# Optimization experiments

Hardware: AMD Instinct MI355X
Metric: run time of the kernel (lower is better)

## Reference

```python
import jax, jax.numpy as jnp
import numpy as np
from jax import lax

B, D, H = 8192, 128, 512   # batch of initial conditions, state dim, MLP width
NSTEPS = 64                # fixed Tsit5 micro-steps over [t0, t1]

# Tsit5 Butcher tableau (Tsitouras 2011), 5th-order solution weights.
A21 = 0.161
A31, A32 = -0.008480655492356989, 0.335480655492357
A41, A42, A43 = 2.8971530571054935, -6.359448489975075, 4.3622954328695815
A51, A52, A53, A54 = 5.325864828439257, -11.748883564062828, 7.4955393428898365, -0.09249506636175525
A61, A62, A63, A64, A65 = 5.86145544294642, -12.92096931784711, 8.159367898576159, -0.071584973281401, -0.028269050394068383
B1, B2, B3, B4, B5, B6 = 0.09646076681806523, 0.01, 0.4798896504144996, 1.379008574103742, -3.290069515436081, 2.324710524099774


def setup_inputs() -> dict:
    key = jax.random.key(0)
    ks = jax.random.split(key, 8)
    s1 = 1.0 / np.sqrt(D)
    s2 = 1.0 / np.sqrt(H)
    return {
        "y0": jax.random.normal(ks[0], (B, D), dtype=jnp.float32),
        "ts": jnp.arange(2, dtype=jnp.float32),  # [0., 1.]
        "W1": jax.random.normal(ks[1], (D, H), dtype=jnp.float32) * s1,
        "b1": jnp.zeros((H,), dtype=jnp.float32),
        "W2": jax.random.normal(ks[2], (H, H), dtype=jnp.float32) * s2,
        "b2": jnp.zeros((H,), dtype=jnp.float32),
        "W3": jax.random.normal(ks[3], (H, D), dtype=jnp.float32) * s2,
        "b3": jnp.zeros((D,), dtype=jnp.float32),
    }


def _mlp(y, W1, b1, W2, b2, W3, b3):
    # autonomous dynamics: f(t, x) = MLP(x)  (t is ignored, as in Dynamics.__call__)
    h = jnp.tanh(y @ W1 + b1)
    h = jnp.tanh(h @ W2 + b2)
    return h @ W3 + b3


def reference(y0, ts, W1, b1, W2, b2, W3, b3):
    dt = (ts[-1] - ts[0]) / NSTEPS
    f = lambda y: _mlp(y, W1, b1, W2, b2, W3, b3)

    def step(y, _):
        k1 = f(y)
        k2 = f(y + dt * (A21 * k1))
        k3 = f(y + dt * (A31 * k1 + A32 * k2))
        k4 = f(y + dt * (A41 * k1 + A42 * k2 + A43 * k3))
        k5 = f(y + dt * (A51 * k1 + A52 * k2 + A53 * k3 + A54 * k4))
        k6 = f(y + dt * (A61 * k1 + A62 * k2 + A63 * k3 + A64 * k4 + A65 * k5))
        y_new = y + dt * (B1 * k1 + B2 * k2 + B3 * k3 + B4 * k4 + B5 * k5 + B6 * k6)
        return y_new, None

    yT, _ = lax.scan(step, y0, None, length=NSTEPS)
    return yT  # solution.ys[-1]: state at t1, shape [B, D]
```

## Files before the change

### kernel.cpp

```cpp
#include <hip/hip_runtime.h>
#include <hip/hip_bf16.h>


#define NSTEPS 64

typedef __attribute__((ext_vector_type(8))) short short8;
typedef __attribute__((ext_vector_type(16))) float f32x16;

static constexpr int OFF_YT   = 0;
static constexpr int OFF_H    = 8192;
static constexpr int KO_S     = 129;
static constexpr int K_BYTES  = 32 * KO_S * 4;
static constexpr int OFF_K0   = 8192 + 32768;
static constexpr int OFF_BIAS = OFF_K0 + 5 * K_BYTES;
static constexpr int SMEM_BYTES = OFF_BIAS + 1152 * 4;

#define C_A21 0.161f
#define C_A31 (-0.008480655492356989f)
#define C_A32 0.335480655492357f
#define C_A41 2.8971530571054935f
#define C_A42 (-6.359448489975075f)
#define C_A43 4.3622954328695815f
#define C_A51 5.325864828439257f
#define C_A52 (-11.748883564062828f)
#define C_A53 7.4955393428898365f
#define C_A54 (-0.09249506636175525f)
#define C_A61 5.86145544294642f
#define C_A62 (-12.92096931784711f)
#define C_A63 8.159367898576159f
#define C_A64 (-0.071584973281401f)
#define C_A65 (-0.028269050394068383f)
#define C_B1 0.09646076681806523f
#define C_B2 0.01f
#define C_B3 0.4798896504144996f
#define C_B4 1.379008574103742f
#define C_B5 (-3.290069515436081f)
#define C_B6 2.324710524099774f

__device__ __forceinline__ float fast_tanh(float x) {
    float e = __builtin_amdgcn_exp2f(x * 2.88539008177792681472f);
    return 1.0f - 2.0f * __builtin_amdgcn_rcpf(e + 1.0f);
}

__device__ __forceinline__ unsigned int pack2(float a, float b) {
    unsigned short lo = __builtin_bit_cast(unsigned short, __float2bfloat16(a));
    unsigned short hi = __builtin_bit_cast(unsigned short, __float2bfloat16(b));
    return ((unsigned int)hi << 16) | (unsigned int)lo;
}

#define MFMA(a, b, c) __builtin_amdgcn_mfma_f32_32x32x16_bf16((a), (b), (c), 0, 0, 0)

__device__ __forceinline__ void store_h(char* smem, int dstOff, const f32x16& acc,
                                        int mt, int q, int lm, const float* bias) {
#pragma unroll
    for (int gblk = 0; gblk < 4; ++gblk) {
        const int r0   = gblk * 4;
        const int row0 = 8 * (r0 >> 2) + 4 * q;
        const int m0   = mt * 32 + row0;
        float v0 = fast_tanh(acc[r0]     + bias[m0]);
        float v1 = fast_tanh(acc[r0 + 1] + bias[m0 + 1]);
        float v2 = fast_tanh(acc[r0 + 2] + bias[m0 + 2]);
        float v3 = fast_tanh(acc[r0 + 3] + bias[m0 + 3]);
        uint2 dw;
        dw.x = pack2(v0, v1);
        dw.y = pack2(v2, v3);
        const int b  = 2 * mt + (r0 >> 3);
        const int s  = lm + 32 * ((r0 >> 2) & 1);
        const int sp = (s + b) & 63;
        *(uint2*)(smem + dstOff + (b << 10) + (sp << 4) + (q << 3)) = dw;
    }
}

__device__ __forceinline__ void write_ytmp(char* smem, int tid, const float* v) {
    const int b  = (tid & 15) >> 1;
    const int s  = (tid >> 4) + 32 * (tid & 1);
    const int sp = (s + b) & 63;
    uint4 pk;
    pk.x = pack2(v[0], v[1]);
    pk.y = pack2(v[2], v[3]);
    pk.z = pack2(v[4], v[5]);
    pk.w = pack2(v[6], v[7]);
    *(uint4*)(smem + OFF_YT + (b << 10) + (sp << 4)) = pk;
}

__device__ __forceinline__ void read_k(const char* smem, int koOff, int tid, float* k) {
    const float* ko = (const float*)(smem + koOff);
    const int kb = (tid >> 4) * KO_S + (tid & 15) * 8;
#pragma unroll
    for (int i = 0; i < 8; ++i) k[i] = ko[kb + i];
}

__device__ __forceinline__ void mlp_eval(char* smem, const uint4* __restrict__ wp,
                                         int tid, int koOff) {
    const int l  = tid & 63;
    const int w  = tid >> 6;
    const int q  = l >> 5;
    const int lm = l & 31;
    const float* sb = (const float*)(smem + OFF_BIAS);

    __syncthreads();

    {
        f32x16 acc0, acc1;
#pragma unroll
        for (int i = 0; i < 16; ++i) { acc0[i] = 0.f; acc1[i] = 0.f; }
        const int mt0 = 2 * w, mt1 = mt0 + 1;
#pragma unroll
        for (int kc = 0; kc < 8; ++kc) {
            short8 bf = *(const short8*)(smem + OFF_YT + (kc << 10) + (((l + kc) & 63) << 4));
            uint4 a0 = wp[(mt0 * 8 + kc) * 64 + l];
            uint4 a1 = wp[(mt1 * 8 + kc) * 64 + l];
            acc0 = MFMA(__builtin_bit_cast(short8, a0), bf, acc0);
            acc1 = MFMA(__builtin_bit_cast(short8, a1), bf, acc1);
        }
        store_h(smem, OFF_H, acc0, mt0, q, lm, sb);
        store_h(smem, OFF_H, acc1, mt1, q, lm, sb);
    }
    __syncthreads();

    {
        f32x16 acc0, acc1;
#pragma unroll
        for (int i = 0; i < 16; ++i) { acc0[i] = 0.f; acc1[i] = 0.f; }
        const int mt0 = 2 * w, mt1 = mt0 + 1;
#pragma unroll 4
        for (int kc = 0; kc < 32; ++kc) {
            short8 bf = *(const short8*)(smem + OFF_H + (kc << 10) + (((l + kc) & 63) << 4));
            uint4 a0 = wp[8192 + (mt0 * 32 + kc) * 64 + l];
            uint4 a1 = wp[8192 + (mt1 * 32 + kc) * 64 + l];
            acc0 = MFMA(__builtin_bit_cast(short8, a0), bf, acc0);
            acc1 = MFMA(__builtin_bit_cast(short8, a1), bf, acc1);
        }
        __syncthreads();
        store_h(smem, OFF_H, acc0, mt0, q, lm, sb + 512);
        store_h(smem, OFF_H, acc1, mt1, q, lm, sb + 512);
    }
    __syncthreads();

    {
        f32x16 acc;
#pragma unroll
        for (int i = 0; i < 16; ++i) acc[i] = 0.f;
        const int mt  = w & 3;
        const int kc0 = (w >> 2) * 16;
#pragma unroll 4
        for (int kk = 0; kk < 16; ++kk) {
            const int kc = kc0 + kk;
            short8 bf = *(const short8*)(smem + OFF_H + (kc << 10) + (((l + kc) & 63) << 4));
            uint4 a = wp[40960 + (mt * 32 + kc) * 64 + l];
            acc = MFMA(__builtin_bit_cast(short8, a), bf, acc);
        }
        float* ko = (float*)(smem + koOff);
        if (w < 4) {
#pragma unroll
            for (int r = 0; r < 16; ++r) {
                const int row = (r & 3) + 8 * (r >> 2) + 4 * q;
                const int df  = mt * 32 + row;
                ko[lm * KO_S + df] = acc[r] + sb[1024 + df];
            }
        }
        __syncthreads();
        if (w >= 4) {
#pragma unroll
            for (int r = 0; r < 16; ++r) {
                const int row = (r & 3) + 8 * (r >> 2) + 4 * q;
                const int df  = mt * 32 + row;
                ko[lm * KO_S + df] += acc[r];
            }
        }
        __syncthreads();
    }
}

__global__ __launch_bounds__(512, 1) void ode_kernel(
    const float* __restrict__ y0, const float* __restrict__ ts,
    const float* __restrict__ b1, const float* __restrict__ b2,
    const float* __restrict__ b3, const uint4* __restrict__ wp,
    float* __restrict__ yout)
{
    extern __shared__ __align__(16) char smem[];
    const int tid = threadIdx.x;
    const int g   = blockIdx.x;

    {
        float* sb = (float*)(smem + OFF_BIAS);
        for (int i = tid; i < 1152; i += 512) {
            float v = (i < 512) ? b1[i] : ((i < 1024) ? b2[i - 512] : b3[i - 1024]);
            sb[i] = v;
        }
    }

    const int row = g * 32 + (tid >> 4);
    const int c0  = (tid & 15) * 8;
    float y[8];
    {
        const float4* src = (const float4*)(y0 + row * 128 + c0);
        float4 v0 = src[0], v1 = src[1];
        y[0] = v0.x; y[1] = v0.y; y[2] = v0.z; y[3] = v0.w;
        y[4] = v1.x; y[5] = v1.y; y[6] = v1.z; y[7] = v1.w;
    }

    const float dt = __builtin_bit_cast(float, __builtin_amdgcn_readfirstlane(
        __builtin_bit_cast(int, (ts[1] - ts[0]) * (1.0f / (float)NSTEPS))));

    float yn[8], yt[8];

    for (int step = 0; step < NSTEPS; ++step) {

        write_ytmp(smem, tid, y);
        mlp_eval(smem, wp, tid, OFF_K0);
        {
            float k1[8];
            read_k(smem, OFF_K0, tid, k1);
#pragma unroll
            for (int i = 0; i < 8; ++i) {
                yn[i] = fmaf(dt, C_B1 * k1[i], y[i]);
                yt[i] = fmaf(dt, C_A21 * k1[i], y[i]);
            }
        }

        write_ytmp(smem, tid, yt);
        mlp_eval(smem, wp, tid, OFF_K0 + K_BYTES);
        {
            float k1[8], k2[8];
            read_k(smem, OFF_K0, tid, k1);
            read_k(smem, OFF_K0 + K_BYTES, tid, k2);
#pragma unroll
            for (int i = 0; i < 8; ++i) {
                yn[i] = fmaf(dt, C_B2 * k2[i], yn[i]);
                yt[i] = fmaf(dt, fmaf(C_A32, k2[i], C_A31 * k1[i]), y[i]);
            }
        }

        write_ytmp(smem, tid, yt);
        mlp_eval(smem, wp, tid, OFF_K0 + 2 * K_BYTES);
        {
            float k1[8], k2[8], k3[8];
            read_k(smem, OFF_K0, tid, k1);
            read_k(smem, OFF_K0 + K_BYTES, tid, k2);
            read_k(smem, OFF_K0 + 2 * K_BYTES, tid, k3);
#pragma unroll
            for (int i = 0; i < 8; ++i) {
                yn[i] = fmaf(dt, C_B3 * k3[i], yn[i]);
                yt[i] = fmaf(dt, fmaf(C_A43, k3[i],
                             fmaf(C_A42, k2[i], C_A41 * k1[i])), y[i]);
            }
        }

        write_ytmp(smem, tid, yt);
        mlp_eval(smem, wp, tid, OFF_K0 + 3 * K_BYTES);
        {
            float k1[8], k2[8], k3[8], k4[8];
            read_k(smem, OFF_K0, tid, k1);
            read_k(smem, OFF_K0 + K_BYTES, tid, k2);
            read_k(smem, OFF_K0 + 2 * K_BYTES, tid, k3);
            read_k(smem, OFF_K0 + 3 * K_BYTES, tid, k4);
#pragma unroll
            for (int i = 0; i < 8; ++i) {
                yn[i] = fmaf(dt, C_B4 * k4[i], yn[i]);
                yt[i] = fmaf(dt, fmaf(C_A54, k4[i], fmaf(C_A53, k3[i],
                             fmaf(C_A52, k2[i], C_A51 * k1[i]))), y[i]);
            }
        }

        write_ytmp(smem, tid, yt);
        mlp_eval(smem, wp, tid, OFF_K0 + 4 * K_BYTES);
        {
            float k1[8], k2[8], k3[8], k4[8], k5[8];
            read_k(smem, OFF_K0, tid, k1);
            read_k(smem, OFF_K0 + K_BYTES, tid, k2);
            read_k(smem, OFF_K0 + 2 * K_BYTES, tid, k3);
            read_k(smem, OFF_K0 + 3 * K_BYTES, tid, k4);
            read_k(smem, OFF_K0 + 4 * K_BYTES, tid, k5);
#pragma unroll
            for (int i = 0; i < 8; ++i) {
                yn[i] = fmaf(dt, C_B5 * k5[i], yn[i]);
                yt[i] = fmaf(dt, fmaf(C_A65, k5[i], fmaf(C_A64, k4[i],
                             fmaf(C_A63, k3[i], fmaf(C_A62, k2[i],
                             C_A61 * k1[i])))), y[i]);
            }
        }

        write_ytmp(smem, tid, yt);
        mlp_eval(smem, wp, tid, OFF_K0);
        {
            float k6[8];
            read_k(smem, OFF_K0, tid, k6);
#pragma unroll
            for (int i = 0; i < 8; ++i) {
                y[i] = fmaf(dt, C_B6 * k6[i], yn[i]);
            }
        }
    }

    {
        float4 o0, o1;
        o0.x = y[0]; o0.y = y[1]; o0.z = y[2]; o0.w = y[3];
        o1.x = y[4]; o1.y = y[5]; o1.z = y[6]; o1.w = y[7];
        float4* dst = (float4*)(yout + row * 128 + c0);
        dst[0] = o0; dst[1] = o1;
    }
}

__global__ void pack_weights(const float* __restrict__ W1, const float* __restrict__ W2,
                             const float* __restrict__ W3, unsigned short* __restrict__ out)
{
    const int tid = blockIdx.x * blockDim.x + threadIdx.x;
    float v;
    if (tid < 65536) {
        const int e = tid, blk = e >> 9, wi = e & 511, l = wi >> 3, j = wi & 7;
        const int mt = blk >> 3, kc = blk & 7;
        const int m = mt * 32 + (l & 31);
        const int k = kc * 16 + 8 * (l >> 5) + j;
        v = W1[k * 512 + m];
    } else if (tid < 327680) {
        const int e = tid - 65536, blk = e >> 9, wi = e & 511, l = wi >> 3, j = wi & 7;
        const int mt = blk >> 5, kc = blk & 31;
        const int m = mt * 32 + (l & 31);
        const int k = kc * 16 + 8 * (l >> 5) + j;
        v = W2[k * 512 + m];
    } else {
        const int e = tid - 327680, blk = e >> 9, wi = e & 511, l = wi >> 3, j = wi & 7;
        const int mt = blk >> 5, kc = blk & 31;
        const int m = mt * 32 + (l & 31);
        const int k = kc * 16 + 8 * (l >> 5) + j;
        v = W3[k * 128 + m];
    }
    out[tid] = __builtin_bit_cast(unsigned short, __float2bfloat16(v));
}

extern "C" void kernel_launch(void* const* d_in, const int* in_sizes, int n_in,
                              void* d_out, int out_size, void* d_ws, size_t ws_size,
                              hipStream_t stream)
{
    const float* y0 = (const float*)d_in[0];
    const float* ts = (const float*)d_in[1];
    const float* W1 = (const float*)d_in[2];
    const float* b1 = (const float*)d_in[3];
    const float* W2 = (const float*)d_in[4];
    const float* b2 = (const float*)d_in[5];
    const float* W3 = (const float*)d_in[6];
    const float* b3 = (const float*)d_in[7];
    unsigned short* wp = (unsigned short*)d_ws;

    pack_weights<<<1536, 256, 0, stream>>>(W1, W2, W3, wp);

    (void)hipFuncSetAttribute((const void*)ode_kernel,
                              hipFuncAttributeMaxDynamicSharedMemorySize, SMEM_BYTES);
    ode_kernel<<<256, 512, SMEM_BYTES, stream>>>(y0, ts, b1, b2, b3,
                                                 (const uint4*)wp, (float*)d_out);
}
```

Measured before the change: 3.567 ms.

## Stream MLP weights via async global-to-LDS DMA with a cross-layer double-buffered pipeline

Weight fragments are no longer loaded from global memory straight into registers right before each MFMA. Each wave now issues global_load_lds DMAs into a private double-buffered LDS staging area, two k-chunks ahead, and the prefetch chain continues across layer boundaries and into the next MLP evaluation. This is meant to hide global/L2 latency behind MFMA work. The __syncthreads calls are replaced by manual lgkmcnt waits plus s_barrier, and the explicit vmcnt/lgkmcnt waits must be exactly right or the code will read stale staging data.

```diff
diff --git a/kernel.cpp b/kernel.cpp
--- a/kernel.cpp
+++ b/kernel.cpp
@@ -13,7 +13,18 @@
 static constexpr int K_BYTES  = 32 * KO_S * 4;
 static constexpr int OFF_K0   = 8192 + 32768;
 static constexpr int OFF_BIAS = OFF_K0 + 5 * K_BYTES;
-static constexpr int SMEM_BYTES = OFF_BIAS + 1152 * 4;
+static constexpr int OFF_ST   = OFF_BIAS + 1152 * 4;
+static constexpr int SMEM_BYTES = OFF_ST + 8 * 4096;
+
+#define W1B(mt, kc) ((mt) * 8 + (kc))
+#define W2B(mt, kc) (128 + (mt) * 32 + (kc))
+#define W3B(mt, kc) (640 + (mt) * 32 + (kc))
+
+#define VMCNT2() asm volatile("s_waitcnt vmcnt(2)" ::: "memory")
+#define VMCNT0() asm volatile("s_waitcnt vmcnt(0)" ::: "memory")
+#define LGKM0()  asm volatile("s_waitcnt lgkmcnt(0)" ::: "memory")
+#define HBAR()   do { LGKM0(); __builtin_amdgcn_s_barrier(); \
+                      asm volatile("" ::: "memory"); } while (0)
 
 #define C_A21 0.161f
 #define C_A31 (-0.008480655492356989f)
@@ -50,6 +61,12 @@
 
 #define MFMA(a, b, c) __builtin_amdgcn_mfma_f32_32x32x16_bf16((a), (b), (c), 0, 0, 0)
 
+__device__ __forceinline__ void dma16(const uint4* __restrict__ g, char* s_) {
+    __builtin_amdgcn_global_load_lds(
+        (const __attribute__((address_space(1))) void*)g,
+        (__attribute__((address_space(3))) void*)s_, 16, 0, 0);
+}
+
 __device__ __forceinline__ void store_h(char* smem, int dstOff, const f32x16& acc,
                                         int mt, int q, int lm, const float* bias) {
 #pragma unroll
@@ -90,85 +107,140 @@
     for (int i = 0; i < 8; ++i) k[i] = ko[kb + i];
 }
 
+#define LD_YT(kc) (*(const short8*)(smem + OFF_YT + ((kc) << 10) + (((l + (kc)) & 63) << 4)))
+#define LD_H(kc)  (*(const short8*)(smem + OFF_H  + ((kc) << 10) + (((l + (kc)) & 63) << 4)))
+
 __device__ __forceinline__ void mlp_eval(char* smem, const uint4* __restrict__ wp,
                                          int tid, int koOff) {
-    const int l  = tid & 63;
-    const int w  = tid >> 6;
-    const int q  = l >> 5;
-    const int lm = l & 31;
+    const int l   = tid & 63;
+    const int w   = tid >> 6;
+    const int q   = l >> 5;
+    const int lm  = l & 31;
+    const int mt0 = 2 * w, mt1 = mt0 + 1;
+    const int mt3 = w & 3, kc03 = (w >> 2) * 16;
     const float* sb = (const float*)(smem + OFF_BIAS);
-
-    __syncthreads();
+    char* stw = smem + OFF_ST + (w << 12);
+
+    HBAR();
+
+    uint4 a0c, a1c, a0n, a1n;
+    short8 bc, bn, b0c, b1c, b0n, b1n;
 
     {
         f32x16 acc0, acc1;
 #pragma unroll
         for (int i = 0; i < 16; ++i) { acc0[i] = 0.f; acc1[i] = 0.f; }
-        const int mt0 = 2 * w, mt1 = mt0 + 1;
-#pragma unroll
-        for (int kc = 0; kc < 8; ++kc) {
-            short8 bf = *(const short8*)(smem + OFF_YT + (kc << 10) + (((l + kc) & 63) << 4));
-            uint4 a0 = wp[(mt0 * 8 + kc) * 64 + l];
-            uint4 a1 = wp[(mt1 * 8 + kc) * 64 + l];
-            acc0 = MFMA(__builtin_bit_cast(short8, a0), bf, acc0);
-            acc1 = MFMA(__builtin_bit_cast(short8, a1), bf, acc1);
+        VMCNT2();
+        a0c = *(const uint4*)(stw + (l << 4));
+        a1c = *(const uint4*)(stw + 1024 + (l << 4));
+        bc  = LD_YT(0);
+#pragma unroll
+        for (int s = 0; s < 8; ++s) {
+            LGKM0();
+            char* ibuf = stw + ((s & 1) << 11);
+            if (s < 6) {
+                dma16(wp + W1B(mt0, s + 2) * 64 + l, ibuf);
+                dma16(wp + W1B(mt1, s + 2) * 64 + l, ibuf + 1024);
+            } else {
+                dma16(wp + W2B(mt0, s - 6) * 64 + l, ibuf);
+                dma16(wp + W2B(mt1, s - 6) * 64 + l, ibuf + 1024);
+            }
+            VMCNT2();
+            char* rbuf = stw + (((s + 1) & 1) << 11);
+            a0n = *(const uint4*)(rbuf + (l << 4));
+            a1n = *(const uint4*)(rbuf + 1024 + (l << 4));
+            if (s < 7) bn = LD_YT(s + 1);
+            acc0 = MFMA(__builtin_bit_cast(short8, a0c), bc, acc0);
+            acc1 = MFMA(__builtin_bit_cast(short8, a1c), bc, acc1);
+            a0c = a0n; a1c = a1n; bc = bn;
         }
         store_h(smem, OFF_H, acc0, mt0, q, lm, sb);
         store_h(smem, OFF_H, acc1, mt1, q, lm, sb);
     }
-    __syncthreads();
+    HBAR();
 
     {
         f32x16 acc0, acc1;
 #pragma unroll
         for (int i = 0; i < 16; ++i) { acc0[i] = 0.f; acc1[i] = 0.f; }
-        const int mt0 = 2 * w, mt1 = mt0 + 1;
+        bc = LD_H(0);
 #pragma unroll 4
-        for (int kc = 0; kc < 32; ++kc) {
-            short8 bf = *(const short8*)(smem + OFF_H + (kc << 10) + (((l + kc) & 63) << 4));
-            uint4 a0 = wp[8192 + (mt0 * 32 + kc) * 64 + l];
-            uint4 a1 = wp[8192 + (mt1 * 32 + kc) * 64 + l];
-            acc0 = MFMA(__builtin_bit_cast(short8, a0), bf, acc0);
-            acc1 = MFMA(__builtin_bit_cast(short8, a1), bf, acc1);
-        }
-        __syncthreads();
+        for (int s2 = 0; s2 < 32; ++s2) {
+            LGKM0();
+            char* ibuf = stw + ((s2 & 1) << 11);
+            if (s2 < 30) {
+                dma16(wp + W2B(mt0, s2 + 2) * 64 + l, ibuf);
+                dma16(wp + W2B(mt1, s2 + 2) * 64 + l, ibuf + 1024);
+            } else {
+                const int j = 2 * (s2 - 30);
+                dma16(wp + W3B(mt3, kc03 + j)     * 64 + l, ibuf);
+                dma16(wp + W3B(mt3, kc03 + j + 1) * 64 + l, ibuf + 1024);
+            }
+            VMCNT2();
+            char* rbuf = stw + (((s2 + 1) & 1) << 11);
+            a0n = *(const uint4*)(rbuf + (l << 4));
+            a1n = *(const uint4*)(rbuf + 1024 + (l << 4));
+            if (s2 < 31) bn = LD_H(s2 + 1);
+            acc0 = MFMA(__builtin_bit_cast(short8, a0c), bc, acc0);
+            acc1 = MFMA(__builtin_bit_cast(short8, a1c), bc, acc1);
+            a0c = a0n; a1c = a1n; bc = bn;
+        }
+        HBAR();
         store_h(smem, OFF_H, acc0, mt0, q, lm, sb + 512);
         store_h(smem, OFF_H, acc1, mt1, q, lm, sb + 512);
     }
-    __syncthreads();
+    HBAR();
 
     {
         f32x16 acc;
 #pragma unroll
         for (int i = 0; i < 16; ++i) acc[i] = 0.f;
-        const int mt  = w & 3;
-        const int kc0 = (w >> 2) * 16;
-#pragma unroll 4
-        for (int kk = 0; kk < 16; ++kk) {
-            const int kc = kc0 + kk;
-            short8 bf = *(const short8*)(smem + OFF_H + (kc << 10) + (((l + kc) & 63) << 4));
-            uint4 a = wp[40960 + (mt * 32 + kc) * 64 + l];
-            acc = MFMA(__builtin_bit_cast(short8, a), bf, acc);
+        b0c = LD_H(kc03);
+        b1c = LD_H(kc03 + 1);
+#pragma unroll
+        for (int s3 = 0; s3 < 8; ++s3) {
+            LGKM0();
+            char* ibuf = stw + ((s3 & 1) << 11);
+            if (s3 < 6) {
+                const int j = 2 * (s3 + 2);
+                dma16(wp + W3B(mt3, kc03 + j)     * 64 + l, ibuf);
+                dma16(wp + W3B(mt3, kc03 + j + 1) * 64 + l, ibuf + 1024);
+            } else {
+                const int kcn = s3 - 6;
+                dma16(wp + W1B(mt0, kcn) * 64 + l, ibuf);
+                dma16(wp + W1B(mt1, kcn) * 64 + l, ibuf + 1024);
+            }
+            VMCNT2();
+            if (s3 < 7) {
+                char* rbuf = stw + (((s3 + 1) & 1) << 11);
+                a0n = *(const uint4*)(rbuf + (l << 4));
+                a1n = *(const uint4*)(rbuf + 1024 + (l << 4));
+                b0n = LD_H(kc03 + 2 * (s3 + 1));
+                b1n = LD_H(kc03 + 2 * (s3 + 1) + 1);
+            }
+            acc = MFMA(__builtin_bit_cast(short8, a0c), b0c, acc);
+            acc = MFMA(__builtin_bit_cast(short8, a1c), b1c, acc);
+            a0c = a0n; a1c = a1n; b0c = b0n; b1c = b1n;
         }
         float* ko = (float*)(smem + koOff);
         if (w < 4) {
 #pragma unroll
             for (int r = 0; r < 16; ++r) {
                 const int row = (r & 3) + 8 * (r >> 2) + 4 * q;
-                const int df  = mt * 32 + row;
+                const int df  = mt3 * 32 + row;
                 ko[lm * KO_S + df] = acc[r] + sb[1024 + df];
             }
         }
-        __syncthreads();
+        HBAR();
         if (w >= 4) {
 #pragma unroll
             for (int r = 0; r < 16; ++r) {
                 const int row = (r & 3) + 8 * (r >> 2) + 4 * q;
-                const int df  = mt * 32 + row;
+                const int df  = mt3 * 32 + row;
                 ko[lm * KO_S + df] += acc[r];
             }
         }
-        __syncthreads();
+        HBAR();
     }
 }
 
@@ -181,6 +253,8 @@
     extern __shared__ __align__(16) char smem[];
     const int tid = threadIdx.x;
     const int g   = blockIdx.x;
+    const int l   = tid & 63;
+    const int w   = tid >> 6;
 
     {
         float* sb = (float*)(smem + OFF_BIAS);
@@ -188,6 +262,15 @@
             float v = (i < 512) ? b1[i] : ((i < 1024) ? b2[i - 512] : b3[i - 1024]);
             sb[i] = v;
         }
+    }
+
+    {
+        char* stw = smem + OFF_ST + (w << 12);
+        const int mt0 = 2 * w, mt1 = mt0 + 1;
+        dma16(wp + W1B(mt0, 0) * 64 + l, stw);
+        dma16(wp + W1B(mt1, 0) * 64 + l, stw + 1024);
+        dma16(wp + W1B(mt0, 1) * 64 + l, stw + 2048);
+        dma16(wp + W1B(mt1, 1) * 64 + l, stw + 2048 + 1024);
     }
 
     const int row = g * 32 + (tid >> 4);
@@ -300,6 +383,8 @@
         float4* dst = (float4*)(yout + row * 128 + c0);
         dst[0] = o0; dst[1] = o1;
     }
+
+    VMCNT0();
 }
 
 __global__ void pack_weights(const float* __restrict__ W1, const float* __restrict__ W2,
```

Result: slower. 4.137 ms (+16.0%).

## Double block to 1024 threads, keep RK stages in registers, atomic-reduce layer 3

Applied to the files above, without the earlier changes.

Raises the block size from 512 to 1024 threads so each wave computes one 32-row M-tile per layer instead of two, and each thread owns four state elements instead of eight. The RK stage vectors k1..k5 now stay in registers instead of being re-read from five shared-memory buffers, so the shared K storage shrinks to a single buffer. The final layer's split-K reduction is done with shared-memory atomicAdd onto a bias-initialised buffer rather than two serialised write and accumulate phases. The aim is more waves to hide MFMA and global weight-load latency, plus fewer barriers and less LDS traffic, at the cost of LDS atomic contention and higher register pressure per wave.

```diff
diff --git a/kernel.cpp b/kernel.cpp
--- a/kernel.cpp
+++ b/kernel.cpp
@@ -10,9 +10,8 @@
 static constexpr int OFF_YT   = 0;
 static constexpr int OFF_H    = 8192;
 static constexpr int KO_S     = 129;
-static constexpr int K_BYTES  = 32 * KO_S * 4;
-static constexpr int OFF_K0   = 8192 + 32768;
-static constexpr int OFF_BIAS = OFF_K0 + 5 * K_BYTES;
+static constexpr int OFF_KO   = 8192 + 32768;
+static constexpr int OFF_BIAS = OFF_KO + 32 * KO_S * 4;
 static constexpr int SMEM_BYTES = OFF_BIAS + 1152 * 4;
 
 #define C_A21 0.161f
@@ -71,27 +70,31 @@
     }
 }
 
-__device__ __forceinline__ void write_ytmp(char* smem, int tid, const float* v) {
-    const int b  = (tid & 15) >> 1;
-    const int s  = (tid >> 4) + 32 * (tid & 1);
-    const int sp = (s + b) & 63;
-    uint4 pk;
+__device__ __forceinline__ void write_ytmp4(char* smem, int tid, const float* v) {
+    const int rowi = tid >> 5;
+    const int d0   = (tid & 31) * 4;
+    const int b    = d0 >> 4;
+    const int h    = (d0 >> 3) & 1;
+    const int s    = rowi + 32 * h;
+    const int sp   = (s + b) & 63;
+    uint2 pk;
     pk.x = pack2(v[0], v[1]);
     pk.y = pack2(v[2], v[3]);
-    pk.z = pack2(v[4], v[5]);
-    pk.w = pack2(v[6], v[7]);
-    *(uint4*)(smem + OFF_YT + (b << 10) + (sp << 4)) = pk;
-}
-
-__device__ __forceinline__ void read_k(const char* smem, int koOff, int tid, float* k) {
-    const float* ko = (const float*)(smem + koOff);
-    const int kb = (tid >> 4) * KO_S + (tid & 15) * 8;
-#pragma unroll
-    for (int i = 0; i < 8; ++i) k[i] = ko[kb + i];
-}
+    *(uint2*)(smem + OFF_YT + (b << 10) + (sp << 4) + ((d0 & 7) << 1)) = pk;
+}
+
+__device__ __forceinline__ void read_k4(const char* smem, int tid, float* k) {
+    const float* ko = (const float*)(smem + OFF_KO);
+    const int kb = (tid >> 5) * KO_S + (tid & 31) * 4;
+#pragma unroll
+    for (int i = 0; i < 4; ++i) k[i] = ko[kb + i];
+}
+
+#define LD_YT(kc) (*(const short8*)(smem + OFF_YT + ((kc) << 10) + (((l + (kc)) & 63) << 4)))
+#define LD_H(kc)  (*(const short8*)(smem + OFF_H  + ((kc) << 10) + (((l + (kc)) & 63) << 4)))
 
 __device__ __forceinline__ void mlp_eval(char* smem, const uint4* __restrict__ wp,
-                                         int tid, int koOff) {
+                                         int tid) {
     const int l  = tid & 63;
     const int w  = tid >> 6;
     const int q  = l >> 5;
@@ -101,39 +104,41 @@
     __syncthreads();
 
     {
-        f32x16 acc0, acc1;
-#pragma unroll
-        for (int i = 0; i < 16; ++i) { acc0[i] = 0.f; acc1[i] = 0.f; }
-        const int mt0 = 2 * w, mt1 = mt0 + 1;
+        f32x16 acc;
+#pragma unroll
+        for (int i = 0; i < 16; ++i) acc[i] = 0.f;
+        const int mt = w;
 #pragma unroll
         for (int kc = 0; kc < 8; ++kc) {
-            short8 bf = *(const short8*)(smem + OFF_YT + (kc << 10) + (((l + kc) & 63) << 4));
-            uint4 a0 = wp[(mt0 * 8 + kc) * 64 + l];
-            uint4 a1 = wp[(mt1 * 8 + kc) * 64 + l];
-            acc0 = MFMA(__builtin_bit_cast(short8, a0), bf, acc0);
-            acc1 = MFMA(__builtin_bit_cast(short8, a1), bf, acc1);
-        }
-        store_h(smem, OFF_H, acc0, mt0, q, lm, sb);
-        store_h(smem, OFF_H, acc1, mt1, q, lm, sb);
+            short8 bf = LD_YT(kc);
+            uint4 a = wp[(mt * 8 + kc) * 64 + l];
+            acc = MFMA(__builtin_bit_cast(short8, a), bf, acc);
+        }
+        store_h(smem, OFF_H, acc, mt, q, lm, sb);
     }
     __syncthreads();
 
     {
-        f32x16 acc0, acc1;
-#pragma unroll
-        for (int i = 0; i < 16; ++i) { acc0[i] = 0.f; acc1[i] = 0.f; }
-        const int mt0 = 2 * w, mt1 = mt0 + 1;
+        f32x16 acc;
+#pragma unroll
+        for (int i = 0; i < 16; ++i) acc[i] = 0.f;
+        const int mt = w;
 #pragma unroll 4
         for (int kc = 0; kc < 32; ++kc) {
-            short8 bf = *(const short8*)(smem + OFF_H + (kc << 10) + (((l + kc) & 63) << 4));
-            uint4 a0 = wp[8192 + (mt0 * 32 + kc) * 64 + l];
-            uint4 a1 = wp[8192 + (mt1 * 32 + kc) * 64 + l];
-            acc0 = MFMA(__builtin_bit_cast(short8, a0), bf, acc0);
-            acc1 = MFMA(__builtin_bit_cast(short8, a1), bf, acc1);
+            short8 bf = LD_H(kc);
+            uint4 a = wp[8192 + (mt * 32 + kc) * 64 + l];
+            acc = MFMA(__builtin_bit_cast(short8, a), bf, acc);
         }
         __syncthreads();
-        store_h(smem, OFF_H, acc0, mt0, q, lm, sb + 512);
-        store_h(smem, OFF_H, acc1, mt1, q, lm, sb + 512);
+        store_h(smem, OFF_H, acc, mt, q, lm, sb + 512);
+
+        {
+            float* ko = (float*)(smem + OFF_KO);
+            const int r = tid >> 5, df0 = (tid & 31) * 4;
+            const float* b3s = sb + 1024;
+#pragma unroll
+            for (int i = 0; i < 4; ++i) ko[r * KO_S + df0 + i] = b3s[df0 + i];
+        }
     }
     __syncthreads();
 
@@ -142,37 +147,26 @@
 #pragma unroll
         for (int i = 0; i < 16; ++i) acc[i] = 0.f;
         const int mt  = w & 3;
-        const int kc0 = (w >> 2) * 16;
+        const int kc0 = (w >> 2) * 8;
 #pragma unroll 4
-        for (int kk = 0; kk < 16; ++kk) {
+        for (int kk = 0; kk < 8; ++kk) {
             const int kc = kc0 + kk;
-            short8 bf = *(const short8*)(smem + OFF_H + (kc << 10) + (((l + kc) & 63) << 4));
+            short8 bf = LD_H(kc);
             uint4 a = wp[40960 + (mt * 32 + kc) * 64 + l];
             acc = MFMA(__builtin_bit_cast(short8, a), bf, acc);
         }
-        float* ko = (float*)(smem + koOff);
-        if (w < 4) {
-#pragma unroll
-            for (int r = 0; r < 16; ++r) {
-                const int row = (r & 3) + 8 * (r >> 2) + 4 * q;
-                const int df  = mt * 32 + row;
-                ko[lm * KO_S + df] = acc[r] + sb[1024 + df];
-            }
+        float* ko = (float*)(smem + OFF_KO);
+#pragma unroll
+        for (int r = 0; r < 16; ++r) {
+            const int row = (r & 3) + 8 * (r >> 2) + 4 * q;
+            const int df  = mt * 32 + row;
+            atomicAdd(&ko[lm * KO_S + df], acc[r]);
         }
         __syncthreads();
-        if (w >= 4) {
-#pragma unroll
-            for (int r = 0; r < 16; ++r) {
-                const int row = (r & 3) + 8 * (r >> 2) + 4 * q;
-                const int df  = mt * 32 + row;
-                ko[lm * KO_S + df] += acc[r];
-            }
-        }
-        __syncthreads();
-    }
-}
-
-__global__ __launch_bounds__(512, 1) void ode_kernel(
+    }
+}
+
+__global__ __launch_bounds__(1024, 4) void ode_kernel(
     const float* __restrict__ y0, const float* __restrict__ ts,
     const float* __restrict__ b1, const float* __restrict__ b2,
     const float* __restrict__ b3, const uint4* __restrict__ wp,
@@ -184,121 +178,93 @@
 
     {
         float* sb = (float*)(smem + OFF_BIAS);
-        for (int i = tid; i < 1152; i += 512) {
+        for (int i = tid; i < 1152; i += 1024) {
             float v = (i < 512) ? b1[i] : ((i < 1024) ? b2[i - 512] : b3[i - 1024]);
             sb[i] = v;
         }
     }
 
-    const int row = g * 32 + (tid >> 4);
-    const int c0  = (tid & 15) * 8;
-    float y[8];
-    {
-        const float4* src = (const float4*)(y0 + row * 128 + c0);
-        float4 v0 = src[0], v1 = src[1];
+    const int row = g * 32 + (tid >> 5);
+    const int c0  = (tid & 31) * 4;
+    float y[4];
+    {
+        float4 v0 = *(const float4*)(y0 + row * 128 + c0);
         y[0] = v0.x; y[1] = v0.y; y[2] = v0.z; y[3] = v0.w;
-        y[4] = v1.x; y[5] = v1.y; y[6] = v1.z; y[7] = v1.w;
     }
 
     const float dt = __builtin_bit_cast(float, __builtin_amdgcn_readfirstlane(
         __builtin_bit_cast(int, (ts[1] - ts[0]) * (1.0f / (float)NSTEPS))));
 
-    float yn[8], yt[8];
+    float yn[4], yt[4];
+    float k1[4], k2[4], k3[4], k4[4], k5[4];
 
     for (int step = 0; step < NSTEPS; ++step) {
 
-        write_ytmp(smem, tid, y);
-        mlp_eval(smem, wp, tid, OFF_K0);
+        write_ytmp4(smem, tid, y);
+        mlp_eval(smem, wp, tid);
+        read_k4(smem, tid, k1);
+#pragma unroll
+        for (int i = 0; i < 4; ++i) {
+            yn[i] = fmaf(dt, C_B1 * k1[i], y[i]);
+            yt[i] = fmaf(dt, C_A21 * k1[i], y[i]);
+        }
+
+        write_ytmp4(smem, tid, yt);
+        mlp_eval(smem, wp, tid);
+        read_k4(smem, tid, k2);
+#pragma unroll
+        for (int i = 0; i < 4; ++i) {
+            yn[i] = fmaf(dt, C_B2 * k2[i], yn[i]);
+            yt[i] = fmaf(dt, fmaf(C_A32, k2[i], C_A31 * k1[i]), y[i]);
+        }
+
+        write_ytmp4(smem, tid, yt);
+        mlp_eval(smem, wp, tid);
+        read_k4(smem, tid, k3);
+#pragma unroll
+        for (int i = 0; i < 4; ++i) {
+            yn[i] = fmaf(dt, C_B3 * k3[i], yn[i]);
+            yt[i] = fmaf(dt, fmaf(C_A43, k3[i],
+                         fmaf(C_A42, k2[i], C_A41 * k1[i])), y[i]);
+        }
+
+        write_ytmp4(smem, tid, yt);
+        mlp_eval(smem, wp, tid);
+        read_k4(smem, tid, k4);
+#pragma unroll
+        for (int i = 0; i < 4; ++i) {
+            yn[i] = fmaf(dt, C_B4 * k4[i], yn[i]);
+            yt[i] = fmaf(dt, fmaf(C_A54, k4[i], fmaf(C_A53, k3[i],
+                         fmaf(C_A52, k2[i], C_A51 * k1[i]))), y[i]);
+        }
+
+        write_ytmp4(smem, tid, yt);
+        mlp_eval(smem, wp, tid);
+        read_k4(smem, tid, k5);
+#pragma unroll
+        for (int i = 0; i < 4; ++i) {
+            yn[i] = fmaf(dt, C_B5 * k5[i], yn[i]);
+            yt[i] = fmaf(dt, fmaf(C_A65, k5[i], fmaf(C_A64, k4[i],
+                         fmaf(C_A63, k3[i], fmaf(C_A62, k2[i],
+                         C_A61 * k1[i])))), y[i]);
+        }
+
+        write_ytmp4(smem, tid, yt);
+        mlp_eval(smem, wp, tid);
         {
-            float k1[8];
-            read_k(smem, OFF_K0, tid, k1);
-#pragma unroll
-            for (int i = 0; i < 8; ++i) {
-                yn[i] = fmaf(dt, C_B1 * k1[i], y[i]);
-                yt[i] = fmaf(dt, C_A21 * k1[i], y[i]);
-            }
-        }
-
-        write_ytmp(smem, tid, yt);
-        mlp_eval(smem, wp, tid, OFF_K0 + K_BYTES);
-        {
-            float k1[8], k2[8];
-            read_k(smem, OFF_K0, tid, k1);
-            read_k(smem, OFF_K0 + K_BYTES, tid, k2);
-#pragma unroll
-            for (int i = 0; i < 8; ++i) {
-                yn[i] = fmaf(dt, C_B2 * k2[i], yn[i]);
-                yt[i] = fmaf(dt, fmaf(C_A32, k2[i], C_A31 * k1[i]), y[i]);
-            }
-        }
-
-        write_ytmp(smem, tid, yt);
-        mlp_eval(smem, wp, tid, OFF_K0 + 2 * K_BYTES);
-        {
-            float k1[8], k2[8], k3[8];
-            read_k(smem, OFF_K0, tid, k1);
-            read_k(smem, OFF_K0 + K_BYTES, tid, k2);
-            read_k(smem, OFF_K0 + 2 * K_BYTES, tid, k3);
-#pragma unroll
-            for (int i = 0; i < 8; ++i) {
-                yn[i] = fmaf(dt, C_B3 * k3[i], yn[i]);
-                yt[i] = fmaf(dt, fmaf(C_A43, k3[i],
-                             fmaf(C_A42, k2[i], C_A41 * k1[i])), y[i]);
-            }
-        }
-
-        write_ytmp(smem, tid, yt);
-        mlp_eval(smem, wp, tid, OFF_K0 + 3 * K_BYTES);
-        {
-            float k1[8], k2[8], k3[8], k4[8];
-            read_k(smem, OFF_K0, tid, k1);
-            read_k(smem, OFF_K0 + K_BYTES, tid, k2);
-            read_k(smem, OFF_K0 + 2 * K_BYTES, tid, k3);
-            read_k(smem, OFF_K0 + 3 * K_BYTES, tid, k4);
-#pragma unroll
-            for (int i = 0; i < 8; ++i) {
-                yn[i] = fmaf(dt, C_B4 * k4[i], yn[i]);
-                yt[i] = fmaf(dt, fmaf(C_A54, k4[i], fmaf(C_A53, k3[i],
-                             fmaf(C_A52, k2[i], C_A51 * k1[i]))), y[i]);
-            }
-        }
-
-        write_ytmp(smem, tid, yt);
-        mlp_eval(smem, wp, tid, OFF_K0 + 4 * K_BYTES);
-        {
-            float k1[8], k2[8], k3[8], k4[8], k5[8];
-            read_k(smem, OFF_K0, tid, k1);
-            read_k(smem, OFF_K0 + K_BYTES, tid, k2);
-            read_k(smem, OFF_K0 + 2 * K_BYTES, tid, k3);
-            read_k(smem, OFF_K0 + 3 * K_BYTES, tid, k4);
-            read_k(smem, OFF_K0 + 4 * K_BYTES, tid, k5);
-#pragma unroll
-            for (int i = 0; i < 8; ++i) {
-                yn[i] = fmaf(dt, C_B5 * k5[i], yn[i]);
-                yt[i] = fmaf(dt, fmaf(C_A65, k5[i], fmaf(C_A64, k4[i],
-                             fmaf(C_A63, k3[i], fmaf(C_A62, k2[i],
-                             C_A61 * k1[i])))), y[i]);
-            }
-        }
-
-        write_ytmp(smem, tid, yt);
-        mlp_eval(smem, wp, tid, OFF_K0);
-        {
-            float k6[8];
-            read_k(smem, OFF_K0, tid, k6);
-#pragma unroll
-            for (int i = 0; i < 8; ++i) {
+            float k6[4];
+            read_k4(smem, tid, k6);
+#pragma unroll
+            for (int i = 0; i < 4; ++i) {
                 y[i] = fmaf(dt, C_B6 * k6[i], yn[i]);
             }
         }
     }
 
     {
-        float4 o0, o1;
-        o0.x = y[0]; o0.y = y[1]; o0.z = y[2]; o0.w = y[3];
-        o1.x = y[4]; o1.y = y[5]; o1.z = y[6]; o1.w = y[7];
-        float4* dst = (float4*)(yout + row * 128 + c0);
-        dst[0] = o0; dst[1] = o1;
+        float4 o;
+        o.x = y[0]; o.y = y[1]; o.z = y[2]; o.w = y[3];
+        *(float4*)(yout + row * 128 + c0) = o;
     }
 }
 
@@ -347,6 +313,6 @@
 
     (void)hipFuncSetAttribute((const void*)ode_kernel,
                               hipFuncAttributeMaxDynamicSharedMemorySize, SMEM_BYTES);
-    ode_kernel<<<256, 512, SMEM_BYTES, stream>>>(y0, ts, b1, b2, b3,
-                                                 (const uint4*)wp, (float*)d_out);
-}
+    ode_kernel<<<256, 1024, SMEM_BYTES, stream>>>(y0, ts, b1, b2, b3,
+                                                  (const uint4*)wp, (float*)d_out);
+}
```

Measured after the change: 11.29 ms. 217% more time.
